# Kernel optimization log

Measured on AMD Instinct MI355X. Metric: run time of the kernel, lower is better.

## Reference

```python
import jax, jax.numpy as jnp
import numpy as np

# --- fan-beam (flat detector) FBP geometry constants, matching init geo dict ---
V, U = 720, 736            # sino_views, nDetecU
NX = NY = 512              # nVoxelX, nVoxelY
SVOX = 400.0               # sVoxelX = sVoxelY (mm)
DU = 1.2858                # dDetecU (mm)
DSO, DOD = 595.0, 490.6    # source-origin, origin-detector distances
DSD = DSO + DOD
DBETA = 2.0 * np.pi / V    # angular step (full 2*pi scan, endpoint=False)


def _ramp_filter_fft():
    """Ram-Lak ramp filter (Kak & Slaney discrete spatial kernel), FFT'd for fast conv."""
    n = np.arange(-(U - 1), U)
    h = np.zeros(2 * U - 1, np.float64)
    h[U - 1] = 1.0 / (4.0 * DU * DU)
    odd = (np.abs(n) % 2 == 1)
    h[odd] = -1.0 / (np.pi * n[odd] * DU) ** 2
    L = int(2 ** np.ceil(np.log2(2 * (2 * U - 1))))  # zero-pad length (linear conv)
    return jnp.asarray(np.fft.fft(h, L).astype(np.complex64)), L

_HF, _L = _ramp_filter_fft()


def setup_inputs() -> dict:
    key = jax.random.key(0)
    sinogram = jax.random.uniform(key, (1, 1, V, U), dtype=jnp.float32)
    return {"sinogram": sinogram}


def reference(sinogram):
    # --- 1) cosine weighting of each detector sample ---
    sino = sinogram.reshape(V, U)
    us = (jnp.arange(U, dtype=jnp.float32) - (U - 1) / 2.0) * DU  # detector coords
    sino_w = sino * (DSD / jnp.sqrt(DSD * DSD + us * us))

    # --- 2) Ram-Lak ramp filtering per view (FFT linear convolution) ---
    Qf = jnp.fft.ifft(jnp.fft.fft(sino_w, n=_L, axis=1) * _HF[None, :], axis=1)
    Q = (jnp.real(Qf)[:, U - 1:2 * U - 1] * DU).astype(jnp.float32)  # [V, U]

    # --- 3) weighted fan-beam backprojection (scan over angles, O(Nx*Ny) carry) ---
    dx = SVOX / NX
    xs = (jnp.arange(NX, dtype=jnp.float32) - (NX - 1) / 2.0) * dx
    X, Y = jnp.meshgrid(xs, xs, indexing='ij')  # [NX, NY]
    betas = jnp.linspace(0.0, 2.0 * np.pi, V, endpoint=False).astype(jnp.float32)

    def body(img, ang_q):
        beta, q = ang_q                       # q: filtered projection [U]
        cb, sb = jnp.cos(beta), jnp.sin(beta)
        t = X * cb + Y * sb                   # coord along detector direction
        s = -X * sb + Y * cb                  # coord toward source
        D = DSO - s                           # source-to-pixel axial distance
        u = DSD * t / D                       # flat-detector intersection (mm)
        idx = u / DU + (U - 1) / 2.0          # fractional detector index
        i0 = jnp.clip(jnp.floor(idx), 0, U - 2).astype(jnp.int32)
        f = idx - i0
        val = q[i0] * (1.0 - f) + q[i0 + 1] * f
        val = jnp.where((idx >= 0.0) & (idx <= U - 1.0), val, 0.0)
        return img + (DSO / D) ** 2 * val, None

    img0 = jnp.zeros((NX, NY), jnp.float32)
    img, _ = jax.lax.scan(body, img0, (betas, Q))
    # 0.5 factor: full 2*pi fan scan covers each ray twice
    return (img * (0.5 * DBETA)).reshape(1, 1, NX, NY)
```

## Files before the change

kernel.cpp:

```cpp
#include <hip/hip_runtime.h>
#include <math.h>

#define NV 720
#define NU 736
#define NUP 768
#define NXY 512

__global__ __launch_bounds__(512) void filter_kernel(const float* __restrict__ sino,
                                                     float* __restrict__ Qi,
                                                     float4* __restrict__ trig,
                                                     float* __restrict__ out_zero) {
    __shared__ float s4[2][368][4];
    __shared__ float wco[736];
    __shared__ float part[3][128][8];
    const int bx = blockIdx.x;
    const int q = bx & 3;
    const int vb = bx >> 2;
    const int v0 = vb * 4;
    const int tid = threadIdx.x;
    const int tz = tid >> 7;
    const int J0 = tid & 127;

    for (int i = bx * 512 + tid; i < NXY * NXY; i += 720 * 512)
        out_zero[i] = 0.0f;

    if (q == 0 && tid < 4) {
        int v = v0 + tid;
        float beta = (float)((double)v * (2.0 * M_PI / 720.0));
        float cb = cosf(beta), sb = sinf(beta);
        const float K = (float)(1085.6 / 1.2858);
        trig[v] = make_float4(cb * K, sb * K, cb, sb);
    }
    const float DSD2 = (float)(1085.6 * 1085.6);
    for (int i = tid; i < 4 * NU; i += 512) {
        const int vv = i / NU, u = i - vv * NU;
        float us = ((float)u - 367.5f) * 1.2858f;
        float cw = 1085.6f / sqrtf(DSD2 + us * us);
        s4[u & 1][u >> 1][vv] = sino[(v0 + vv) * NU + u] * cw;
    }
    for (int i = tid; i < 736; i += 512) {
        double n = (double)(2 * i - 735);
        double a = M_PI * n * 1.2858;
        wco[i] = (float)(-1.0 / (a * a));
    }
    __syncthreads();

    const int m0 = 92 * tz;
    float a00 = 0.f, a01 = 0.f, a02 = 0.f, a03 = 0.f;
    float a10 = 0.f, a11 = 0.f, a12 = 0.f, a13 = 0.f;
    const int J0c = min(J0, 91);
    const int y0 = J0c + 367 + 92 * q;
    const float* wp = &wco[y0 - m0];

    #pragma unroll 4
    for (int mm = 0; mm < 92; ++mm) {
        const int m = m0 + mm;
        const float w0 = wp[-mm];
        const float w1 = wp[1 - mm];
        const float4 sv1 = *(const float4*)&s4[1][m][0];
        const float4 sv0 = *(const float4*)&s4[0][m][0];
        a00 = fmaf(w0, sv1.x, a00); a01 = fmaf(w0, sv1.y, a01);
        a02 = fmaf(w0, sv1.z, a02); a03 = fmaf(w0, sv1.w, a03);
        a10 = fmaf(w1, sv0.x, a10); a11 = fmaf(w1, sv0.y, a11);
        a12 = fmaf(w1, sv0.z, a12); a13 = fmaf(w1, sv0.w, a13);
    }

    if (tz != 0 && J0 < 92) {
        *(float4*)&part[tz - 1][J0][0] = make_float4(a00, a01, a02, a03);
        *(float4*)&part[tz - 1][J0][4] = make_float4(a10, a11, a12, a13);
    }
    __syncthreads();

    if (tz == 0 && J0 < 92) {
        #pragma unroll
        for (int g = 0; g < 3; ++g) {
            const float4 p0 = *(const float4*)&part[g][J0][0];
            const float4 p1 = *(const float4*)&part[g][J0][4];
            a00 += p0.x; a01 += p0.y; a02 += p0.z; a03 += p0.w;
            a10 += p1.x; a11 += p1.y; a12 += p1.z; a13 += p1.w;
        }
        const float H0 = (float)(1.0 / (4.0 * 1.2858 * 1.2858));
        const int mc = J0 + 92 * q;
        const float4 c0 = *(const float4*)&s4[0][mc][0];
        const float4 c1 = *(const float4*)&s4[1][mc][0];
        a00 = fmaf(H0, c0.x, a00); a01 = fmaf(H0, c0.y, a01);
        a02 = fmaf(H0, c0.z, a02); a03 = fmaf(H0, c0.w, a03);
        a10 = fmaf(H0, c1.x, a10); a11 = fmaf(H0, c1.y, a11);
        a12 = fmaf(H0, c1.z, a12); a13 = fmaf(H0, c1.w, a13);
        const int j0i = 2 * mc;
        const float DU = 1.2858f;
        const int v180 = v0 % 180;
        const int wq = v0 / 180;
        float* qr = Qi + (size_t)v180 * 3072 + wq;
        qr[0 * 3072 + 4 * j0i]       = a00 * DU;  qr[0 * 3072 + 4 * (j0i + 1)] = a10 * DU;
        qr[1 * 3072 + 4 * j0i]       = a01 * DU;  qr[1 * 3072 + 4 * (j0i + 1)] = a11 * DU;
        qr[2 * 3072 + 4 * j0i]       = a02 * DU;  qr[2 * 3072 + 4 * (j0i + 1)] = a12 * DU;
        qr[3 * 3072 + 4 * j0i]       = a03 * DU;  qr[3 * 3072 + 4 * (j0i + 1)] = a13 * DU;
    }
}

__global__ __launch_bounds__(256) void bp_kernel(const float* __restrict__ Qi,
                                                 const float4* __restrict__ trig,
                                                 float* __restrict__ out) {
    __shared__ float win[2][4][NUP];
    const int b = blockIdx.x;
    const int c = b & 15;
    const int blk = b >> 4;
    const int bx = blk >> 4;
    const int by = blk & 15;
    const int t = threadIdx.x;
    const int w = t >> 6;
    const int l = t & 63;
    const int iq = (bx << 4) + ((w >> 1) << 3) + (l >> 3);
    const int jq = (by << 4) + ((w & 1) << 3) + (l & 7);

    const float dx = 400.0f / 512.0f;
    const float X = ((float)iq - 255.5f) * dx;
    const float Y = ((float)jq - 255.5f) * dx;
    const float Kc = (float)(1085.6 / 1.2858);

    float acc0 = 0.0f, acc1 = 0.0f, acc2 = 0.0f, acc3 = 0.0f;
    const bool inr = fmaf(X, X, Y * Y) <= 236.5f * 236.5f;
    const bool myint = __all(inr);

    const int nk = (c < 4) ? 12 : 11;
    const float* rowp = Qi + (size_t)c * 3072;
    const float4* tvp = trig + c;

    #pragma unroll
    for (int ch = 0; ch < 3; ++ch)
        __builtin_amdgcn_global_load_lds(
            (const __attribute__((address_space(1))) void*)(rowp + w * 768 + ch * 256 + l * 4),
            (__attribute__((address_space(3))) void*)&win[0][w][ch * 256],
            16, 0, 0);

    for (int it = 0; it < nk; ++it) {
        __syncthreads();
        if (it + 1 < nk) {
            const float* rn = rowp + 16 * 3072;
            #pragma unroll
            for (int ch = 0; ch < 3; ++ch)
                __builtin_amdgcn_global_load_lds(
                    (const __attribute__((address_space(1))) void*)(rn + w * 768 + ch * 256 + l * 4),
                    (__attribute__((address_space(3))) void*)&win[(it + 1) & 1][w][ch * 256],
                    16, 0, 0);
        }
        const float* winf = &win[it & 1][0][0];

        __builtin_amdgcn_s_setprio(1);
        if (myint) {
            const float4 tv = tvp[0];
            float a = fmaf(tv.z, X, tv.w * Y);
            float bb = fmaf(tv.z, Y, -tv.w * X);
            float aK = a * Kc, bK = bb * Kc;
            float D0 = 595.0f - bb, D1 = 595.0f + a, D2 = 595.0f + bb, D3 = 595.0f - a;
            float r0 = __builtin_amdgcn_rcpf(D0);
            float r1 = __builtin_amdgcn_rcpf(D1);
            float r2 = __builtin_amdgcn_rcpf(D2);
            float r3 = __builtin_amdgcn_rcpf(D3);
            float fi0 = fmaf(aK,  r0, 367.5f);
            float fi1 = fmaf(bK,  r1, 367.5f);
            float fi2 = fmaf(-aK, r2, 367.5f);
            float fi3 = fmaf(-bK, r3, 367.5f);
            int im[4] = {(int)fi0, (int)fi1, (int)fi2, (int)fi3};
            float ff[4] = {__builtin_amdgcn_fractf(fi0), __builtin_amdgcn_fractf(fi1),
                           __builtin_amdgcn_fractf(fi2), __builtin_amdgcn_fractf(fi3)};
            float gg[4] = {r0 * r0, r1 * r1, r2 * r2, r3 * r3};
            float* accp[4] = {&acc0, &acc1, &acc2, &acc3};
            #pragma unroll
            for (int m = 0; m < 4; ++m) {
                const float* pm = winf + 4 * im[m];
                #pragma unroll
                for (int k = 0; k < 4; ++k) {
                    float q0 = pm[k];
                    float q1 = pm[k + 4];
                    float val = fmaf(ff[m], q1 - q0, q0);
                    *accp[(m - k) & 3] = fmaf(gg[m], val, *accp[(m - k) & 3]);
                }
            }
        } else {
            const float4 tvs[4] = {tvp[0], tvp[180], tvp[360], tvp[540]};
            const float pX[4] = {X, Y, -X, -Y};
            const float pY[4] = {Y, -X, -Y, X};
            float* accp[4] = {&acc0, &acc1, &acc2, &acc3};
            #pragma unroll
            for (int j = 0; j < 4; ++j) {
                float Xm = pX[j], Ym = pY[j];
                #pragma unroll
                for (int k = 0; k < 4; ++k) {
                    const float4 tv = tvs[k];
                    float t2 = fmaf(tv.x, Xm, tv.y * Ym);
                    float D  = fmaf(tv.w, Xm, fmaf(tv.z, -Ym, 595.0f));
                    float rD = __builtin_amdgcn_rcpf(D);
                    float fidx = fmaf(t2, rD, 367.5f);
                    int i0c = min(max((int)fidx, 0), NU - 2);
                    float f = __builtin_amdgcn_fractf(fidx);
                    const float* pe = winf + 4 * i0c;
                    float q0 = pe[k];
                    float q1 = pe[k + 4];
                    float val = fmaf(f, q1 - q0, q0);
                    float cen = fidx - 367.5f;
                    float g = (__builtin_fabsf(cen) <= 367.5f) ? rD * rD : 0.0f;
                    *accp[j] = fmaf(g, val, *accp[j]);
                }
            }
        }
        __builtin_amdgcn_s_setprio(0);
        rowp += 16 * 3072;
        tvp += 16;
    }
    const float SC = (float)(595.0 * 595.0 * 0.5 * (2.0 * M_PI / 720.0));
    const int ir = 511 - iq, jr = 511 - jq;
    unsafeAtomicAdd(&out[iq * NXY + jq], acc0 * SC);
    unsafeAtomicAdd(&out[jq * NXY + ir], acc1 * SC);
    unsafeAtomicAdd(&out[ir * NXY + jr], acc2 * SC);
    unsafeAtomicAdd(&out[jr * NXY + iq], acc3 * SC);
}

extern "C" void kernel_launch(void* const* d_in, const int* in_sizes, int n_in,
                              void* d_out, int out_size, void* d_ws, size_t ws_size,
                              hipStream_t stream) {
    const float* sino = (const float*)d_in[0];
    float* out = (float*)d_out;
    float* Qi = (float*)d_ws;
    float4* trig = (float4*)((char*)d_ws + (size_t)180 * 3072 * sizeof(float));

    filter_kernel<<<720, 512, 0, stream>>>(sino, Qi, trig, out);
    bp_kernel<<<4096, 256, 0, stream>>>(Qi, trig, out);
}
```

Measured before the change: 108.3 us.

## Store filtered projections as fp16 and interpolate with packed half math

The filter kernel now writes the interleaved filtered projections as _Float16 instead of float, halving the workspace row size and the LDS window in the backprojection kernel. The backprojection loads half as much data per iteration through global_load_lds and, in the interior path, does the linear interpolation with packed half2 arithmetic before converting to float for accumulation. This targets memory/LDS bandwidth and ALU count in the hot loop, at the cost of reduced precision in filtered values and interpolation weights, which may affect accuracy tolerance.

```diff
diff --git a/kernel.cpp b/kernel.cpp
--- a/kernel.cpp
+++ b/kernel.cpp
@@ -3,8 +3,10 @@
 
 #define NV 720
 #define NU 736
-#define NUP 768
 #define NXY 512
+#define ROWD 1536
+
+typedef _Float16 h2v __attribute__((ext_vector_type(2)));
 
 __global__ __launch_bounds__(512) void filter_kernel(const float* __restrict__ sino,
                                                      float* __restrict__ Qi,
@@ -90,19 +92,24 @@
         const int j0i = 2 * mc;
         const float DU = 1.2858f;
         const int v180 = v0 % 180;
-        const int wq = v0 / 180;
-        float* qr = Qi + (size_t)v180 * 3072 + wq;
-        qr[0 * 3072 + 4 * j0i]       = a00 * DU;  qr[0 * 3072 + 4 * (j0i + 1)] = a10 * DU;
-        qr[1 * 3072 + 4 * j0i]       = a01 * DU;  qr[1 * 3072 + 4 * (j0i + 1)] = a11 * DU;
-        qr[2 * 3072 + 4 * j0i]       = a02 * DU;  qr[2 * 3072 + 4 * (j0i + 1)] = a12 * DU;
-        qr[3 * 3072 + 4 * j0i]       = a03 * DU;  qr[3 * 3072 + 4 * (j0i + 1)] = a13 * DU;
+        const int s = v0 / 180;
+        _Float16* qh = (_Float16*)Qi;
+        const int h0 = 4 * j0i + s;
+        qh[(size_t)(v180 + 0) * (ROWD * 2) + h0]     = (_Float16)(a00 * DU);
+        qh[(size_t)(v180 + 0) * (ROWD * 2) + h0 + 4] = (_Float16)(a10 * DU);
+        qh[(size_t)(v180 + 1) * (ROWD * 2) + h0]     = (_Float16)(a01 * DU);
+        qh[(size_t)(v180 + 1) * (ROWD * 2) + h0 + 4] = (_Float16)(a11 * DU);
+        qh[(size_t)(v180 + 2) * (ROWD * 2) + h0]     = (_Float16)(a02 * DU);
+        qh[(size_t)(v180 + 2) * (ROWD * 2) + h0 + 4] = (_Float16)(a12 * DU);
+        qh[(size_t)(v180 + 3) * (ROWD * 2) + h0]     = (_Float16)(a03 * DU);
+        qh[(size_t)(v180 + 3) * (ROWD * 2) + h0 + 4] = (_Float16)(a13 * DU);
     }
 }
 
 __global__ __launch_bounds__(256) void bp_kernel(const float* __restrict__ Qi,
                                                  const float4* __restrict__ trig,
                                                  float* __restrict__ out) {
-    __shared__ float win[2][4][NUP];
+    __shared__ __align__(16) unsigned int win[2][ROWD];
     const int b = blockIdx.x;
     const int c = b & 15;
     const int blk = b >> 4;
@@ -124,28 +131,31 @@
     const bool myint = __all(inr);
 
     const int nk = (c < 4) ? 12 : 11;
-    const float* rowp = Qi + (size_t)c * 3072;
+    const unsigned int* rowp = (const unsigned int*)Qi + (size_t)c * ROWD;
     const float4* tvp = trig + c;
 
-    #pragma unroll
-    for (int ch = 0; ch < 3; ++ch)
+    __builtin_amdgcn_global_load_lds(
+        (const __attribute__((address_space(1))) void*)(rowp + w * 256 + l * 4),
+        (__attribute__((address_space(3))) void*)&win[0][w * 256], 16, 0, 0);
+    if (w < 2)
         __builtin_amdgcn_global_load_lds(
-            (const __attribute__((address_space(1))) void*)(rowp + w * 768 + ch * 256 + l * 4),
-            (__attribute__((address_space(3))) void*)&win[0][w][ch * 256],
-            16, 0, 0);
+            (const __attribute__((address_space(1))) void*)(rowp + 1024 + w * 256 + l * 4),
+            (__attribute__((address_space(3))) void*)&win[0][1024 + w * 256], 16, 0, 0);
 
     for (int it = 0; it < nk; ++it) {
         __syncthreads();
         if (it + 1 < nk) {
-            const float* rn = rowp + 16 * 3072;
-            #pragma unroll
-            for (int ch = 0; ch < 3; ++ch)
+            const unsigned int* rn = rowp + 16 * ROWD;
+            unsigned int* wn = &win[(it + 1) & 1][0];
+            __builtin_amdgcn_global_load_lds(
+                (const __attribute__((address_space(1))) void*)(rn + w * 256 + l * 4),
+                (__attribute__((address_space(3))) void*)&wn[w * 256], 16, 0, 0);
+            if (w < 2)
                 __builtin_amdgcn_global_load_lds(
-                    (const __attribute__((address_space(1))) void*)(rn + w * 768 + ch * 256 + l * 4),
-                    (__attribute__((address_space(3))) void*)&win[(it + 1) & 1][w][ch * 256],
-                    16, 0, 0);
+                    (const __attribute__((address_space(1))) void*)(rn + 1024 + w * 256 + l * 4),
+                    (__attribute__((address_space(3))) void*)&wn[1024 + w * 256], 16, 0, 0);
         }
-        const float* winf = &win[it & 1][0][0];
+        const unsigned int* winf = &win[it & 1][0];
 
         __builtin_amdgcn_s_setprio(1);
         if (myint) {
@@ -169,14 +179,22 @@
             float* accp[4] = {&acc0, &acc1, &acc2, &acc3};
             #pragma unroll
             for (int m = 0; m < 4; ++m) {
-                const float* pm = winf + 4 * im[m];
+                const uint2* pm = (const uint2*)(winf + 2 * im[m]);
+                const uint2 A = pm[0];
+                const uint2 B = pm[1];
+                h2v a01 = __builtin_bit_cast(h2v, A.x);
+                h2v a23 = __builtin_bit_cast(h2v, A.y);
+                h2v b01 = __builtin_bit_cast(h2v, B.x);
+                h2v b23 = __builtin_bit_cast(h2v, B.y);
+                const _Float16 fh = (_Float16)ff[m];
+                const h2v fv = {fh, fh};
+                const h2v v01 = (b01 - a01) * fv + a01;
+                const h2v v23 = (b23 - a23) * fv + a23;
+                const float vv_[4] = {(float)v01.x, (float)v01.y,
+                                      (float)v23.x, (float)v23.y};
                 #pragma unroll
-                for (int k = 0; k < 4; ++k) {
-                    float q0 = pm[k];
-                    float q1 = pm[k + 4];
-                    float val = fmaf(ff[m], q1 - q0, q0);
-                    *accp[(m - k) & 3] = fmaf(gg[m], val, *accp[(m - k) & 3]);
-                }
+                for (int k = 0; k < 4; ++k)
+                    *accp[(m - k) & 3] = fmaf(gg[m], vv_[k], *accp[(m - k) & 3]);
             }
         } else {
             const float4 tvs[4] = {tvp[0], tvp[180], tvp[360], tvp[540]};
@@ -195,9 +213,13 @@
                     float fidx = fmaf(t2, rD, 367.5f);
                     int i0c = min(max((int)fidx, 0), NU - 2);
                     float f = __builtin_amdgcn_fractf(fidx);
-                    const float* pe = winf + 4 * i0c;
-                    float q0 = pe[k];
-                    float q1 = pe[k + 4];
+                    const int d = 2 * i0c + (k >> 1);
+                    const unsigned int w0 = winf[d];
+                    const unsigned int w1 = winf[d + 2];
+                    h2v h0 = __builtin_bit_cast(h2v, w0);
+                    h2v h1 = __builtin_bit_cast(h2v, w1);
+                    float q0 = (k & 1) ? (float)h0.y : (float)h0.x;
+                    float q1 = (k & 1) ? (float)h1.y : (float)h1.x;
                     float val = fmaf(f, q1 - q0, q0);
                     float cen = fidx - 367.5f;
                     float g = (__builtin_fabsf(cen) <= 367.5f) ? rD * rD : 0.0f;
@@ -206,7 +228,7 @@
             }
         }
         __builtin_amdgcn_s_setprio(0);
-        rowp += 16 * 3072;
+        rowp += 16 * ROWD;
         tvp += 16;
     }
     const float SC = (float)(595.0 * 595.0 * 0.5 * (2.0 * M_PI / 720.0));
@@ -223,7 +245,7 @@
     const float* sino = (const float*)d_in[0];
     float* out = (float*)d_out;
     float* Qi = (float*)d_ws;
-    float4* trig = (float4*)((char*)d_ws + (size_t)180 * 3072 * sizeof(float));
+    float4* trig = (float4*)((char*)d_ws + (size_t)180 * ROWD * sizeof(unsigned int));
 
     filter_kernel<<<720, 512, 0, stream>>>(sino, Qi, trig, out);
     bp_kernel<<<4096, 256, 0, stream>>>(Qi, trig, out);
```

New measurement: 109.9 us. About the same (+1.5%).
